# Kernel optimization log

Measured on AMD Instinct MI355X. Metric: run time of the kernel, lower is better.

The kernel has to match this reference:

```python
import jax, jax.numpy as jnp
import numpy as np

N_NODES = 100000
N_EDGES = 1600000
IN_DIM = 128
OUT_DIM = 128


def setup_inputs() -> dict:
    key = jax.random.key(0)
    k_x, k_r, k_c, k_v, k_w, k_b = jax.random.split(key, 6)
    x = jax.random.normal(k_x, (N_NODES, IN_DIM), dtype=jnp.float32)
    rows = jax.random.randint(k_r, (N_EDGES,), 0, N_NODES, dtype=jnp.int32)
    cols = jax.random.randint(k_c, (N_EDGES,), 0, N_NODES, dtype=jnp.int32)
    vals = jax.random.uniform(k_v, (N_EDGES,), dtype=jnp.float32)
    # nn.Linear(in_dim, out_dim): kaiming-uniform-ish init, exact values irrelevant
    bound = 1.0 / np.sqrt(IN_DIM)
    W = jax.random.uniform(k_w, (IN_DIM, OUT_DIM), dtype=jnp.float32, minval=-bound, maxval=bound)
    b = jax.random.uniform(k_b, (OUT_DIM,), dtype=jnp.float32, minval=-bound, maxval=bound)
    return {"x": x, "W": W, "b": b, "vals": vals, "rows": rows, "cols": cols}


def reference(x, W, b, vals, rows, cols):
    # x = self.linear(x)
    h = x @ W + b  # [N, out_dim]
    # x = torch.sparse.mm(adj, x): out[r] += vals[e] * h[cols[e]] for each edge e with rows[e]==r
    msgs = vals[:, None] * h[cols]  # [E, out_dim]
    out = jax.ops.segment_sum(msgs, rows, num_segments=N_NODES)  # [N, out_dim]
    return out
```

## Files before the change

kernel.cpp:

```cpp
#include <hip/hip_runtime.h>

#define N_NODES 100000
#define N_EDGES 1600000
#define DIM 128
#define NBKT 782
#define CAP  2300
#define CAPL 2304
#define B1   256
#define EPB  6250
#define GEMM_NB 1563

typedef __attribute__((ext_vector_type(8))) short bf16x8;
typedef __attribute__((ext_vector_type(4))) float f32x4;

__device__ __forceinline__ unsigned short f2bf(float f) {
    unsigned u = __float_as_uint(f);
    u += 0x7FFF + ((u >> 16) & 1);
    return (unsigned short)(u >> 16);
}
__device__ __forceinline__ float bflo(unsigned u) { return __uint_as_float(u << 16); }
__device__ __forceinline__ float bfhi(unsigned u) { return __uint_as_float(u & 0xFFFF0000u); }

__global__ __launch_bounds__(256) void wt_pack(const float* __restrict__ W,
                                               uint4* __restrict__ wtf,
                                               int* __restrict__ gcur) {
    const int t = blockIdx.x * 256 + threadIdx.x;
    if (t < NBKT) gcur[t * 4] = t * CAP;
    const int f = t >> 6;
    const int l = t & 63;
    const int kc = f >> 3, nt = f & 7;
    const int quad = l >> 4, n = l & 15;
    unsigned o[4];
    #pragma unroll
    for (int jj = 0; jj < 4; ++jj) {
        const int k0 = kc * 32 + quad * 8 + jj * 2;
        const unsigned short lo = f2bf(W[(k0 + 0) * DIM + nt * 16 + n]);
        const unsigned short hi = f2bf(W[(k0 + 1) * DIM + nt * 16 + n]);
        o[jj] = (unsigned)lo | ((unsigned)hi << 16);
    }
    wtf[t] = make_uint4(o[0], o[1], o[2], o[3]);
}

#define ROWSTRIDE 136
__global__ __launch_bounds__(256) void gemm_scatter(const float* __restrict__ x,
                                                    const uint4* __restrict__ wtf,
                                                    const float* __restrict__ b,
                                                    unsigned short* __restrict__ h,
                                                    const int* __restrict__ rows,
                                                    const int* __restrict__ cols,
                                                    const float* __restrict__ vals,
                                                    int* __restrict__ gcur,
                                                    int2* __restrict__ binned) {
    __shared__ uint4 smem4[4 * 16 * ROWSTRIDE / 8];
    if (blockIdx.x >= GEMM_NB) {
        int* c   = (int*)smem4;
        int* cur = c + NBKT;
        const int k = blockIdx.x - GEMM_NB, t = threadIdx.x;
        for (int bb = t; bb < NBKT; bb += 256) c[bb] = 0;
        __syncthreads();
        const int e0 = k * EPB;
        #pragma unroll
        for (int i = 0; i < 6; ++i) {
            const int4 r4 = *(const int4*)&rows[e0 + (t + i * 256) * 4];
            atomicAdd(&c[r4.x >> 7], 1);
            atomicAdd(&c[r4.y >> 7], 1);
            atomicAdd(&c[r4.z >> 7], 1);
            atomicAdd(&c[r4.w >> 7], 1);
        }
        if (t < EPB - 6144) atomicAdd(&c[rows[e0 + 6144 + t] >> 7], 1);
        __syncthreads();
        for (int bb = t; bb < NBKT; bb += 256) {
            const int cc = c[bb];
            if (cc) cur[bb] = atomicAdd(&gcur[bb * 4], cc);
        }
        __syncthreads();
        #pragma unroll
        for (int i = 0; i < 6; ++i) {
            const int g = (t + i * 256) * 4;
            const int4   r4 = *(const int4*)&rows[e0 + g];
            const int4   c4 = *(const int4*)&cols[e0 + g];
            const float4 v4 = *(const float4*)&vals[e0 + g];
            int bb, p;
            bb = r4.x >> 7; p = atomicAdd(&cur[bb], 1);
            if (p < (bb + 1) * CAP) binned[p] = make_int2(((r4.x & 127) << 24) | c4.x, __float_as_int(v4.x));
            bb = r4.y >> 7; p = atomicAdd(&cur[bb], 1);
            if (p < (bb + 1) * CAP) binned[p] = make_int2(((r4.y & 127) << 24) | c4.y, __float_as_int(v4.y));
            bb = r4.z >> 7; p = atomicAdd(&cur[bb], 1);
            if (p < (bb + 1) * CAP) binned[p] = make_int2(((r4.z & 127) << 24) | c4.z, __float_as_int(v4.z));
            bb = r4.w >> 7; p = atomicAdd(&cur[bb], 1);
            if (p < (bb + 1) * CAP) binned[p] = make_int2(((r4.w & 127) << 24) | c4.w, __float_as_int(v4.w));
        }
        if (t < EPB - 6144) {
            const int e = e0 + 6144 + t;
            const int r = rows[e];
            const int bb = r >> 7;
            const int p = atomicAdd(&cur[bb], 1);
            if (p < (bb + 1) * CAP) binned[p] = make_int2(((r & 127) << 24) | cols[e], __float_as_int(vals[e]));
        }
        return;
    }

    const int wave = threadIdx.x >> 6;
    const int lane = threadIdx.x & 63;
    const int quad = lane >> 4;
    const int m = lane & 15;
    const int row_base = blockIdx.x * 64 + wave * 16;
    const int row = row_base + m;
    const bool rok = (row < N_NODES);

    uint4 bf[32];
    #pragma unroll
    for (int f = 0; f < 32; ++f) bf[f] = wtf[f * 64 + lane];

    bf16x8 af[4];
    #pragma unroll
    for (int kc = 0; kc < 4; ++kc) {
        float4 v0, v1;
        if (rok) {
            v0 = *(const float4*)&x[(size_t)row * DIM + kc * 32 + quad * 8];
            v1 = *(const float4*)&x[(size_t)row * DIM + kc * 32 + quad * 8 + 4];
        } else {
            v0 = make_float4(0.f, 0.f, 0.f, 0.f);
            v1 = make_float4(0.f, 0.f, 0.f, 0.f);
        }
        union { bf16x8 v; unsigned u[4]; } a;
        a.u[0] = (unsigned)f2bf(v0.x) | ((unsigned)f2bf(v0.y) << 16);
        a.u[1] = (unsigned)f2bf(v0.z) | ((unsigned)f2bf(v0.w) << 16);
        a.u[2] = (unsigned)f2bf(v1.x) | ((unsigned)f2bf(v1.y) << 16);
        a.u[3] = (unsigned)f2bf(v1.z) | ((unsigned)f2bf(v1.w) << 16);
        af[kc] = a.v;
    }

    f32x4 acc[8];
    #pragma unroll
    for (int nt = 0; nt < 8; ++nt) {
        const float bv = b[nt * 16 + m];
        acc[nt] = (f32x4){bv, bv, bv, bv};
    }

    #pragma unroll
    for (int kc = 0; kc < 4; ++kc) {
        #pragma unroll
        for (int nt = 0; nt < 8; ++nt) {
            union { uint4 u; bf16x8 v; } bb; bb.u = bf[kc * 8 + nt];
            acc[nt] = __builtin_amdgcn_mfma_f32_16x16x32_bf16(af[kc], bb.v, acc[nt], 0, 0, 0);
        }
    }

    unsigned short* sh = (unsigned short*)smem4 + wave * 16 * ROWSTRIDE;
    #pragma unroll
    for (int nt = 0; nt < 8; ++nt) {
        #pragma unroll
        for (int i = 0; i < 4; ++i)
            sh[(quad * 4 + i) * ROWSTRIDE + nt * 16 + m] = f2bf(acc[nt][i]);
    }
    __syncthreads();
    uint4* hv4 = (uint4*)h;
    const int seg = lane & 15;
    #pragma unroll
    for (int c = 0; c < 4; ++c) {
        const int rl = (lane >> 4) + c * 4;
        const int r = row_base + rl;
        const uint4 v = *(const uint4*)&sh[rl * ROWSTRIDE + seg * 8];
        if (r < N_NODES) hv4[(size_t)r * 16 + seg] = v;
    }
}

__global__ __launch_bounds__(512) void p2_gather(const unsigned* __restrict__ h32,
                                                 const int2* __restrict__ binned,
                                                 const int* __restrict__ gcur,
                                                 float* __restrict__ out) {
    __shared__ int2 ebuf[CAPL];
    __shared__ int rcount[128], rstart[128], rcur[128], sscan[128];
    const int b = blockIdx.x, t = threadIdx.x;
    const int s0 = b * CAP;
    int n = gcur[b * 4] - s0;
    if (n > CAPL) n = CAPL;

    int2 ereg[5];
    int nm = 0;
    #pragma unroll
    for (int jj = 0; jj < 5; ++jj) {
        const int j = t + jj * 512;
        if (j < n) { ereg[jj] = binned[s0 + j]; nm = jj + 1; }
    }

    if (t < 128) rcount[t] = 0;
    __syncthreads();
    #pragma unroll
    for (int jj = 0; jj < 5; ++jj)
        if (jj < nm) atomicAdd(&rcount[((unsigned)ereg[jj].x) >> 24], 1);
    __syncthreads();

    if (t < 128) sscan[t] = rcount[t];
    __syncthreads();
    for (int o = 1; o < 128; o <<= 1) {
        const int add = (t < 128 && t >= o) ? sscan[t - o] : 0;
        __syncthreads();
        if (t < 128) sscan[t] += add;
        __syncthreads();
    }
    if (t < 128) { rstart[t] = sscan[t] - rcount[t]; rcur[t] = sscan[t] - rcount[t]; }
    __syncthreads();

    #pragma unroll
    for (int jj = 0; jj < 5; ++jj)
        if (jj < nm) {
            const int lr = ((unsigned)ereg[jj].x) >> 24;
            const int pos = atomicAdd(&rcur[lr], 1);
            ebuf[pos] = make_int2(ereg[jj].x & 0x00FFFFFF, ereg[jj].y);
        }
    __syncthreads();

    const int wave = t >> 6, lane = t & 63;
    const char* hbase = (const char*)h32;
    const unsigned lane4 = (unsigned)lane * 4u;

    for (int i = 0; i < 8; ++i) {
        const int lr0 = wave * 16 + i;
        const int lr1 = lr0 + 8;
        const int r0 = b * 128 + lr0;
        const int r1 = b * 128 + lr1;
        const int st0 = rstart[lr0], cn0 = rcount[lr0];
        const int st1 = rstart[lr1], cn1 = rcount[lr1];

        float a0x = 0.f, a0y = 0.f, c0x = 0.f, c0y = 0.f;
        float a1x = 0.f, a1y = 0.f, c1x = 0.f, c1y = 0.f;
        int j0 = 0, j1 = 0;

        while (j0 + 2 <= cn0 && j1 + 2 <= cn1) {
            const int2 e0 = ebuf[st0 + j0], e1 = ebuf[st0 + j0 + 1];
            const int2 f0 = ebuf[st1 + j1], f1 = ebuf[st1 + j1 + 1];
            const unsigned u0 = *(const unsigned*)(hbase + ((((unsigned)e0.x) << 8) | lane4));
            const unsigned u1 = *(const unsigned*)(hbase + ((((unsigned)e1.x) << 8) | lane4));
            const unsigned w0 = *(const unsigned*)(hbase + ((((unsigned)f0.x) << 8) | lane4));
            const unsigned w1 = *(const unsigned*)(hbase + ((((unsigned)f1.x) << 8) | lane4));
            const float v0 = __int_as_float(e0.y), v1 = __int_as_float(e1.y);
            const float s0v = __int_as_float(f0.y), s1v = __int_as_float(f1.y);
            a0x = fmaf(v0, bflo(u0), a0x);  a0y = fmaf(v0, bfhi(u0), a0y);
            c0x = fmaf(v1, bflo(u1), c0x);  c0y = fmaf(v1, bfhi(u1), c0y);
            a1x = fmaf(s0v, bflo(w0), a1x); a1y = fmaf(s0v, bfhi(w0), a1y);
            c1x = fmaf(s1v, bflo(w1), c1x); c1y = fmaf(s1v, bfhi(w1), c1y);
            j0 += 2; j1 += 2;
        }
        for (; j0 + 2 <= cn0; j0 += 2) {
            const int2 e0 = ebuf[st0 + j0], e1 = ebuf[st0 + j0 + 1];
            const unsigned u0 = *(const unsigned*)(hbase + ((((unsigned)e0.x) << 8) | lane4));
            const unsigned u1 = *(const unsigned*)(hbase + ((((unsigned)e1.x) << 8) | lane4));
            const float v0 = __int_as_float(e0.y), v1 = __int_as_float(e1.y);
            a0x = fmaf(v0, bflo(u0), a0x); a0y = fmaf(v0, bfhi(u0), a0y);
            c0x = fmaf(v1, bflo(u1), c0x); c0y = fmaf(v1, bfhi(u1), c0y);
        }
        if (j0 < cn0) {
            const int2 e0 = ebuf[st0 + j0];
            const unsigned u0 = *(const unsigned*)(hbase + ((((unsigned)e0.x) << 8) | lane4));
            const float v0 = __int_as_float(e0.y);
            a0x = fmaf(v0, bflo(u0), a0x); a0y = fmaf(v0, bfhi(u0), a0y);
        }
        for (; j1 + 2 <= cn1; j1 += 2) {
            const int2 f0 = ebuf[st1 + j1], f1 = ebuf[st1 + j1 + 1];
            const unsigned w0 = *(const unsigned*)(hbase + ((((unsigned)f0.x) << 8) | lane4));
            const unsigned w1 = *(const unsigned*)(hbase + ((((unsigned)f1.x) << 8) | lane4));
            const float s0v = __int_as_float(f0.y), s1v = __int_as_float(f1.y);
            a1x = fmaf(s0v, bflo(w0), a1x); a1y = fmaf(s0v, bfhi(w0), a1y);
            c1x = fmaf(s1v, bflo(w1), c1x); c1y = fmaf(s1v, bfhi(w1), c1y);
        }
        if (j1 < cn1) {
            const int2 f0 = ebuf[st1 + j1];
            const unsigned w0 = *(const unsigned*)(hbase + ((((unsigned)f0.x) << 8) | lane4));
            const float s0v = __int_as_float(f0.y);
            a1x = fmaf(s0v, bflo(w0), a1x); a1y = fmaf(s0v, bfhi(w0), a1y);
        }

        if (r0 < N_NODES) {
            float2 o; o.x = a0x + c0x; o.y = a0y + c0y;
            *(float2*)&out[(size_t)r0 * DIM + lane * 2] = o;
        }
        if (r1 < N_NODES) {
            float2 o; o.x = a1x + c1x; o.y = a1y + c1y;
            *(float2*)&out[(size_t)r1 * DIM + lane * 2] = o;
        }
    }
}

extern "C" void kernel_launch(void* const* d_in, const int* in_sizes, int n_in,
                              void* d_out, int out_size, void* d_ws, size_t ws_size,
                              hipStream_t stream) {
    const float* x    = (const float*)d_in[0];
    const float* W    = (const float*)d_in[1];
    const float* b    = (const float*)d_in[2];
    const float* vals = (const float*)d_in[3];
    const int*   rows = (const int*)d_in[4];
    const int*   cols = (const int*)d_in[5];
    float* out = (float*)d_out;

    char* ws = (char*)d_ws;
    unsigned short* h = (unsigned short*)(ws + 0);
    uint4* wtf    = (uint4*)(ws + 25600000);
    int*   gcur   = (int*)  (ws + 25632768);
    int2*  binned = (int2*) (ws + 25645280);

    wt_pack<<<8, 256, 0, stream>>>(W, wtf, gcur);

    gemm_scatter<<<GEMM_NB + B1, 256, 0, stream>>>(x, wtf, b, h, rows, cols, vals,
                                                   gcur, binned);

    p2_gather<<<NBKT, 512, 0, stream>>>((const unsigned*)h, binned, gcur, out);
}
```

Baseline: 220.1 us.

## Move binning blocks first, use smaller edge chunks, split gather buckets across two blocks

The binning blocks now come first in the fused grid, so edge scattering starts early instead of trailing the GEMM blocks. Each binning block handles fewer edges (2560 instead of 6250), which spreads the work over more blocks. The gather kernel now runs two 256-thread blocks per 128-row bucket, one per half. Each block filters the bucket's edges down to its 64 rows and scans the row counts with wave shuffles. This gives smaller per-block LDS use and more parallelism, at the cost of each bucket's binned entries being read twice.

```diff
diff --git a/kernel.cpp b/kernel.cpp
--- a/kernel.cpp
+++ b/kernel.cpp
@@ -5,9 +5,9 @@
 #define DIM 128
 #define NBKT 782
 #define CAP  2300
-#define CAPL 2304
-#define B1   256
-#define EPB  6250
+#define CAPH 1248
+#define B1   625
+#define EPB  2560
 #define GEMM_NB 1563
 
 typedef __attribute__((ext_vector_type(8))) short bf16x8;
@@ -52,22 +52,28 @@
                                                     int* __restrict__ gcur,
                                                     int2* __restrict__ binned) {
     __shared__ uint4 smem4[4 * 16 * ROWSTRIDE / 8];
-    if (blockIdx.x >= GEMM_NB) {
+    if (blockIdx.x < B1) {
         int* c   = (int*)smem4;
         int* cur = c + NBKT;
-        const int k = blockIdx.x - GEMM_NB, t = threadIdx.x;
+        const int k = blockIdx.x, t = threadIdx.x;
         for (int bb = t; bb < NBKT; bb += 256) c[bb] = 0;
         __syncthreads();
         const int e0 = k * EPB;
         #pragma unroll
-        for (int i = 0; i < 6; ++i) {
+        for (int i = 0; i < 2; ++i) {
             const int4 r4 = *(const int4*)&rows[e0 + (t + i * 256) * 4];
             atomicAdd(&c[r4.x >> 7], 1);
             atomicAdd(&c[r4.y >> 7], 1);
             atomicAdd(&c[r4.z >> 7], 1);
             atomicAdd(&c[r4.w >> 7], 1);
         }
-        if (t < EPB - 6144) atomicAdd(&c[rows[e0 + 6144 + t] >> 7], 1);
+        if (t < 128) {
+            const int4 r4 = *(const int4*)&rows[e0 + 2048 + t * 4];
+            atomicAdd(&c[r4.x >> 7], 1);
+            atomicAdd(&c[r4.y >> 7], 1);
+            atomicAdd(&c[r4.z >> 7], 1);
+            atomicAdd(&c[r4.w >> 7], 1);
+        }
         __syncthreads();
         for (int bb = t; bb < NBKT; bb += 256) {
             const int cc = c[bb];
@@ -75,11 +81,11 @@
         }
         __syncthreads();
         #pragma unroll
-        for (int i = 0; i < 6; ++i) {
-            const int g = (t + i * 256) * 4;
-            const int4   r4 = *(const int4*)&rows[e0 + g];
-            const int4   c4 = *(const int4*)&cols[e0 + g];
-            const float4 v4 = *(const float4*)&vals[e0 + g];
+        for (int i = 0; i < 2; ++i) {
+            const int g = e0 + (t + i * 256) * 4;
+            const int4   r4 = *(const int4*)&rows[g];
+            const int4   c4 = *(const int4*)&cols[g];
+            const float4 v4 = *(const float4*)&vals[g];
             int bb, p;
             bb = r4.x >> 7; p = atomicAdd(&cur[bb], 1);
             if (p < (bb + 1) * CAP) binned[p] = make_int2(((r4.x & 127) << 24) | c4.x, __float_as_int(v4.x));
@@ -90,21 +96,30 @@
             bb = r4.w >> 7; p = atomicAdd(&cur[bb], 1);
             if (p < (bb + 1) * CAP) binned[p] = make_int2(((r4.w & 127) << 24) | c4.w, __float_as_int(v4.w));
         }
-        if (t < EPB - 6144) {
-            const int e = e0 + 6144 + t;
-            const int r = rows[e];
-            const int bb = r >> 7;
-            const int p = atomicAdd(&cur[bb], 1);
-            if (p < (bb + 1) * CAP) binned[p] = make_int2(((r & 127) << 24) | cols[e], __float_as_int(vals[e]));
+        if (t < 128) {
+            const int g = e0 + 2048 + t * 4;
+            const int4   r4 = *(const int4*)&rows[g];
+            const int4   c4 = *(const int4*)&cols[g];
+            const float4 v4 = *(const float4*)&vals[g];
+            int bb, p;
+            bb = r4.x >> 7; p = atomicAdd(&cur[bb], 1);
+            if (p < (bb + 1) * CAP) binned[p] = make_int2(((r4.x & 127) << 24) | c4.x, __float_as_int(v4.x));
+            bb = r4.y >> 7; p = atomicAdd(&cur[bb], 1);
+            if (p < (bb + 1) * CAP) binned[p] = make_int2(((r4.y & 127) << 24) | c4.y, __float_as_int(v4.y));
+            bb = r4.z >> 7; p = atomicAdd(&cur[bb], 1);
+            if (p < (bb + 1) * CAP) binned[p] = make_int2(((r4.z & 127) << 24) | c4.z, __float_as_int(v4.z));
+            bb = r4.w >> 7; p = atomicAdd(&cur[bb], 1);
+            if (p < (bb + 1) * CAP) binned[p] = make_int2(((r4.w & 127) << 24) | c4.w, __float_as_int(v4.w));
         }
         return;
     }
 
+    const int bid = blockIdx.x - B1;
     const int wave = threadIdx.x >> 6;
     const int lane = threadIdx.x & 63;
     const int quad = lane >> 4;
     const int m = lane & 15;
-    const int row_base = blockIdx.x * 64 + wave * 16;
+    const int row_base = bid * 64 + wave * 16;
     const int row = row_base + m;
     const bool rok = (row < N_NODES);
 
@@ -166,61 +181,71 @@
     }
 }
 
-__global__ __launch_bounds__(512) void p2_gather(const unsigned* __restrict__ h32,
+__global__ __launch_bounds__(256) void p2_gather(const unsigned* __restrict__ h32,
                                                  const int2* __restrict__ binned,
                                                  const int* __restrict__ gcur,
                                                  float* __restrict__ out) {
-    __shared__ int2 ebuf[CAPL];
-    __shared__ int rcount[128], rstart[128], rcur[128], sscan[128];
-    const int b = blockIdx.x, t = threadIdx.x;
-    const int s0 = b * CAP;
-    int n = gcur[b * 4] - s0;
-    if (n > CAPL) n = CAPL;
-
-    int2 ereg[5];
-    int nm = 0;
-    #pragma unroll
-    for (int jj = 0; jj < 5; ++jj) {
-        const int j = t + jj * 512;
-        if (j < n) { ereg[jj] = binned[s0 + j]; nm = jj + 1; }
-    }
-
-    if (t < 128) rcount[t] = 0;
-    __syncthreads();
-    #pragma unroll
-    for (int jj = 0; jj < 5; ++jj)
-        if (jj < nm) atomicAdd(&rcount[((unsigned)ereg[jj].x) >> 24], 1);
-    __syncthreads();
-
-    if (t < 128) sscan[t] = rcount[t];
-    __syncthreads();
-    for (int o = 1; o < 128; o <<= 1) {
-        const int add = (t < 128 && t >= o) ? sscan[t - o] : 0;
-        __syncthreads();
-        if (t < 128) sscan[t] += add;
-        __syncthreads();
-    }
-    if (t < 128) { rstart[t] = sscan[t] - rcount[t]; rcur[t] = sscan[t] - rcount[t]; }
-    __syncthreads();
-
-    #pragma unroll
-    for (int jj = 0; jj < 5; ++jj)
-        if (jj < nm) {
-            const int lr = ((unsigned)ereg[jj].x) >> 24;
-            const int pos = atomicAdd(&rcur[lr], 1);
-            ebuf[pos] = make_int2(ereg[jj].x & 0x00FFFFFF, ereg[jj].y);
+    __shared__ int2 ebuf[CAPH];
+    __shared__ int rcount[64], rstart[64], rcur[64];
+    const int blk = blockIdx.x, t = threadIdx.x;
+    const int B = blk >> 1, hf = blk & 1;
+    const int s0 = B * CAP;
+    int n = gcur[B * 4] - s0;
+    if (n > CAP) n = CAP;
+
+    int2 ereg[9];
+    int lrh[9];
+    #pragma unroll
+    for (int jj = 0; jj < 9; ++jj) lrh[jj] = -1;
+    if (t < 64) rcount[t] = 0;
+    __syncthreads();
+    #pragma unroll
+    for (int jj = 0; jj < 9; ++jj) {
+        const int j = t + jj * 256;
+        if (j < n) {
+            const int2 e = binned[s0 + j];
+            const int lr = ((unsigned)e.x) >> 24;
+            if ((lr >> 6) == hf) {
+                ereg[jj] = e;
+                lrh[jj] = lr & 63;
+                atomicAdd(&rcount[lr & 63], 1);
+            }
+        }
+    }
+    __syncthreads();
+
+    if (t < 64) {
+        const int c0 = rcount[t];
+        int v = c0;
+        #pragma unroll
+        for (int o = 1; o < 64; o <<= 1) {
+            const int u = __shfl_up(v, o, 64);
+            if (t >= o) v += u;
+        }
+        rstart[t] = v - c0;
+        rcur[t] = v - c0;
+    }
+    __syncthreads();
+
+    #pragma unroll
+    for (int jj = 0; jj < 9; ++jj)
+        if (lrh[jj] >= 0) {
+            const int pos = atomicAdd(&rcur[lrh[jj]], 1);
+            if (pos < CAPH)
+                ebuf[pos] = make_int2(ereg[jj].x & 0x00FFFFFF, ereg[jj].y);
         }
     __syncthreads();
 
     const int wave = t >> 6, lane = t & 63;
     const char* hbase = (const char*)h32;
     const unsigned lane4 = (unsigned)lane * 4u;
+    const int row_base = B * 128 + hf * 64;
 
     for (int i = 0; i < 8; ++i) {
         const int lr0 = wave * 16 + i;
         const int lr1 = lr0 + 8;
-        const int r0 = b * 128 + lr0;
-        const int r1 = b * 128 + lr1;
+        const int r0 = row_base + lr0;
+        const int r1 = row_base + lr1;
         const int st0 = rstart[lr0], cn0 = rcount[lr0];
         const int st1 = rstart[lr1], cn1 = rcount[lr1];
 
@@ -302,8 +327,8 @@
 
     wt_pack<<<8, 256, 0, stream>>>(W, wtf, gcur);
 
-    gemm_scatter<<<GEMM_NB + B1, 256, 0, stream>>>(x, wtf, b, h, rows, cols, vals,
+    gemm_scatter<<<B1 + GEMM_NB, 256, 0, stream>>>(x, wtf, b, h, rows, cols, vals,
                                                    gcur, binned);
 
-    p2_gather<<<NBKT, 512, 0, stream>>>((const unsigned*)h, binned, gcur, out);
-}
+    p2_gather<<<2 * NBKT, 256, 0, stream>>>((const unsigned*)h, binned, gcur, out);
+}
```

Measured after the change: 221.7 us. No clear change (+0.7%).
